# Performance work log

Measured on AMD Instinct MI355X. Metric: run time of the kernel, lower is better.

## Reference

```python
import jax, jax.numpy as jnp
import numpy as np

T, B, V, H = 512, 1024, 64, 100  # seq_len, batch, vocab(output_size), hidden_size


def setup_inputs() -> dict:
    key = jax.random.key(0)
    ks = jax.random.split(key, 9)
    s = 0.1
    x = jax.random.uniform(ks[0], (T, B, V), dtype=jnp.float32)  # teacher-forced inputs (one-hot-like floats)
    h = jax.random.normal(ks[1], (1, B, H), dtype=jnp.float32)   # encoder final hidden
    lens = jax.random.randint(ks[2], (B,), 1, T + 1, dtype=jnp.int32)
    lengths = jnp.sort(lens)[::-1]          # descending, packed-sequence order
    lengths = lengths.at[0].set(T)          # max length == T (batch_sizes[0] == B)
    W_ih = jax.random.normal(ks[3], (3 * H, V), dtype=jnp.float32) * s
    W_hh = jax.random.normal(ks[4], (3 * H, H), dtype=jnp.float32) * s
    b_ih = jax.random.normal(ks[5], (3 * H,), dtype=jnp.float32) * s
    b_hh = jax.random.normal(ks[6], (3 * H,), dtype=jnp.float32) * s
    W_out = jax.random.normal(ks[7], (V, H), dtype=jnp.float32) * s
    b_out = jax.random.normal(ks[8], (V,), dtype=jnp.float32) * s
    return dict(x=x, h=h, lengths=lengths, W_ih=W_ih, W_hh=W_hh,
                b_ih=b_ih, b_hh=b_hh, W_out=W_out, b_out=b_out)


def gru_cell(x_t, h_t, W_ih, W_hh, b_ih, b_hh):
    # PyTorch nn.GRUCell math, gate order (r, z, n)
    gi = x_t @ W_ih.T + b_ih   # [B, 3H]
    gh = h_t @ W_hh.T + b_hh   # [B, 3H]
    i_r, i_z, i_n = jnp.split(gi, 3, axis=-1)
    h_r, h_z, h_n = jnp.split(gh, 3, axis=-1)
    r = jax.nn.sigmoid(i_r + h_r)
    z = jax.nn.sigmoid(i_z + h_z)
    n = jnp.tanh(i_n + r * h_n)
    return (1.0 - z) * n + z * h_t


def reference(x, h, lengths, W_ih, W_hh, b_ih, b_hh, W_out, b_out):
    # Packed-sequence GRUCell decode with full teacher forcing (forcing_ratio=1.0).
    # Padded emulation: at step t only rows with t < length are active
    # (== first batch_sizes[t] rows in packed order since lengths are descending).
    hidden0 = h[0]                                          # [B, H]
    mask = jnp.arange(T)[:, None] < lengths[None, :]        # [T, B]

    def step(hidden, inp):
        x_t, m = inp
        h_new = gru_cell(x_t, hidden, W_ih, W_hh, b_ih, b_hh)
        hidden = jnp.where(m[:, None], h_new, hidden)
        logp = jax.nn.log_softmax(hidden @ W_out.T + b_out, axis=-1)  # [B, V]
        return hidden, jnp.where(m[:, None], logp, 0.0)

    _, outputs = jax.lax.scan(step, hidden0, (x, mask))
    return outputs  # [T, B, V] log-probs, zero at padded positions
```

## Files before the change

kernel.cpp:

```cpp
#include <hip/hip_runtime.h>


#define T_STEPS 512
#define BATCH   1024
#define VOCAB   64
#define HID     100
#define BB      16
#define NKH     4
#define NKX     2
#define HSTR    136
#define LSTR    68

typedef _Float16 f16;
typedef _Float16 f16x8 __attribute__((ext_vector_type(8)));
typedef float    f32x4 __attribute__((ext_vector_type(4)));

#define MFMA(A_, B_, C_) __builtin_amdgcn_mfma_f32_16x16x32_f16((A_), (B_), (C_), 0, 0, 0)

__device__ __forceinline__ float sigm(float v)   { return 1.0f / (1.0f + __expf(-v)); }
__device__ __forceinline__ float tanh_f(float v) { return 1.0f - 2.0f / (__expf(2.0f * v) + 1.0f); }

__global__ __launch_bounds__(512, 2) void gru_mfma(
    const float* __restrict__ x, const float* __restrict__ h0,
    const int* __restrict__ lengths,
    const float* __restrict__ W_ih, const float* __restrict__ W_hh,
    const float* __restrict__ b_ih, const float* __restrict__ b_hh,
    const float* __restrict__ W_out, const float* __restrict__ b_out,
    float* __restrict__ out)
{
    const int tid = threadIdx.x;
    const int w   = tid >> 6;
    const int l   = tid & 63;
    const int c   = l & 15;
    const int lg  = l >> 4;
    const int rowbase = blockIdx.x * BB;

    __shared__ alignas(16) f16   hHi[2][BB * HSTR];
    __shared__ alignas(16) f16   hLo[2][BB * HSTR];
    __shared__ alignas(16) float logitsL[BB * LSTR];
    __shared__ int lensL[BB];

    f16x8 wf[18];
    float bin = 0.f;
    float hold4[4];
    int   lenv[4];

    #pragma unroll
    for (int r = 0; r < 4; ++r) lenv[r] = lengths[rowbase + lg * 4 + r];

    if (w < 7) {
        const int gl = 16 * w + c;
        const bool gv = gl < HID;
        #pragma unroll
        for (int s = 0; s < 3; ++s) {
            const int g = s * HID + gl;
            #pragma unroll
            for (int ks = 0; ks < NKH; ++ks) {
                f16x8 v;
                #pragma unroll
                for (int j = 0; j < 8; ++j) {
                    const int k = ks * 32 + lg * 8 + j;
                    float val = 0.f;
                    if (gv) {
                        if (k < HID)        val = W_hh[(size_t)g * HID + k];
                        else if (k == HID)  val = (s < 2) ? (b_ih[g] + b_hh[g]) : b_hh[g];
                    }
                    v[j] = (f16)val;
                }
                wf[s * 4 + ks] = v;
            }
            #pragma unroll
            for (int ks = 0; ks < NKX; ++ks) {
                f16x8 v;
                #pragma unroll
                for (int j = 0; j < 8; ++j) {
                    const int k = ks * 32 + lg * 8 + j;
                    v[j] = (f16)(gv ? W_ih[(size_t)g * VOCAB + k] : 0.f);
                }
                wf[12 + s * 2 + ks] = v;
            }
        }
        bin = gv ? b_ih[2 * HID + gl] : 0.f;

        #pragma unroll
        for (int r = 0; r < 4; ++r) {
            const int row = lg * 4 + r;
            float hv = gv ? h0[(size_t)(rowbase + row) * HID + gl] : 0.f;
            hold4[r] = hv;
            if (gv) {
                f16 hi = (f16)hv;
                hHi[0][row * HSTR + gl] = hi;
                hLo[0][row * HSTR + gl] = (f16)(hv - (float)hi);
            }
        }
    } else {
        #pragma unroll
        for (int vt = 0; vt < 4; ++vt) {
            const int vr = 16 * vt + c;
            #pragma unroll
            for (int ks = 0; ks < NKH; ++ks) {
                f16x8 v;
                #pragma unroll
                for (int j = 0; j < 8; ++j) {
                    const int k = ks * 32 + lg * 8 + j;
                    float val = 0.f;
                    if (k < HID)        val = W_out[(size_t)vr * HID + k];
                    else if (k == HID)  val = b_out[vr];
                    v[j] = (f16)val;
                }
                wf[vt * 4 + ks] = v;
            }
        }
        hold4[0] = hold4[1] = hold4[2] = hold4[3] = 0.f;
    }

    if (tid < BB) {
        lensL[tid] = lengths[rowbase + tid];
        #pragma unroll
        for (int k = HID; k < 128; ++k) {
            hHi[0][tid * HSTR + k] = (f16)0.f;  hLo[0][tid * HSTR + k] = (f16)0.f;
            hHi[1][tid * HSTR + k] = (f16)0.f;  hLo[1][tid * HSTR + k] = (f16)0.f;
        }
        hHi[0][tid * HSTR + HID] = (f16)1.0f;
        hHi[1][tid * HSTR + HID] = (f16)1.0f;
    }

    f16x8 xf[NKX];
    if (w < 7) {
        const float* xp = x + ((size_t)rowbase + c) * VOCAB + lg * 8;
        #pragma unroll
        for (int ks = 0; ks < NKX; ++ks) {
            float4 a  = *reinterpret_cast<const float4*>(xp + ks * 32);
            float4 b2 = *reinterpret_cast<const float4*>(xp + ks * 32 + 4);
            f16x8 v;
            v[0] = (f16)a.x;  v[1] = (f16)a.y;  v[2] = (f16)a.z;  v[3] = (f16)a.w;
            v[4] = (f16)b2.x; v[5] = (f16)b2.y; v[6] = (f16)b2.z; v[7] = (f16)b2.w;
            xf[ks] = v;
        }
    }
    __syncthreads();

    for (int t = 0; t <= T_STEPS; ++t) {
        const int cur = t & 1;
        if (w < 7) {
            if (t < T_STEPS) {
                const int tn = (t + 1 < T_STEPS) ? t + 1 : t;
                const float* xp = x + ((size_t)tn * BATCH + rowbase + c) * VOCAB + lg * 8;
                float4 xp0 = *reinterpret_cast<const float4*>(xp);
                float4 xp1 = *reinterpret_cast<const float4*>(xp + 4);
                float4 xp2 = *reinterpret_cast<const float4*>(xp + 32);
                float4 xp3 = *reinterpret_cast<const float4*>(xp + 36);

                f16x8 hh[NKH], hl[NKH];
                #pragma unroll
                for (int ks = 0; ks < NKH; ++ks) {
                    const int off = c * HSTR + ks * 32 + lg * 8;
                    hh[ks] = *reinterpret_cast<const f16x8*>(&hHi[cur][off]);
                    hl[ks] = *reinterpret_cast<const f16x8*>(&hLo[cur][off]);
                }

                f32x4 aR = {0.f,0.f,0.f,0.f}, aZ = aR, aNX = aR, aNH = aR;
                #pragma unroll
                for (int ks = 0; ks < NKX; ++ks) {
                    aR  = MFMA(xf[ks], wf[12 + ks], aR);
                    aZ  = MFMA(xf[ks], wf[14 + ks], aZ);
                    aNX = MFMA(xf[ks], wf[16 + ks], aNX);
                }
                #pragma unroll
                for (int ks = 0; ks < NKH; ++ks) {
                    aR  = MFMA(hl[ks], wf[0 + ks], aR);
                    aR  = MFMA(hh[ks], wf[0 + ks], aR);
                    aZ  = MFMA(hl[ks], wf[4 + ks], aZ);
                    aZ  = MFMA(hh[ks], wf[4 + ks], aZ);
                    aNH = MFMA(hl[ks], wf[8 + ks], aNH);
                    aNH = MFMA(hh[ks], wf[8 + ks], aNH);
                }

                const int kk = 16 * w + c;
                const bool kv = kk < HID;
                #pragma unroll
                for (int r = 0; r < 4; ++r) {
                    float rg   = sigm(aR[r]);
                    float zg   = sigm(aZ[r]);
                    float ng   = tanh_f(fmaf(rg, aNH[r], aNX[r] + bin));
                    float hnew = fmaf(zg, hold4[r] - ng, ng);
                    float hv   = (t < lenv[r]) ? hnew : hold4[r];
                    hold4[r] = hv;
                    if (kv) {
                        const int row = lg * 4 + r;
                        f16 hi = (f16)hv;
                        hHi[cur ^ 1][row * HSTR + kk] = hi;
                        hLo[cur ^ 1][row * HSTR + kk] = (f16)(hv - (float)hi);
                    }
                }

                f16x8 v;
                v[0] = (f16)xp0.x; v[1] = (f16)xp0.y; v[2] = (f16)xp0.z; v[3] = (f16)xp0.w;
                v[4] = (f16)xp1.x; v[5] = (f16)xp1.y; v[6] = (f16)xp1.z; v[7] = (f16)xp1.w;
                xf[0] = v;
                v[0] = (f16)xp2.x; v[1] = (f16)xp2.y; v[2] = (f16)xp2.z; v[3] = (f16)xp2.w;
                v[4] = (f16)xp3.x; v[5] = (f16)xp3.y; v[6] = (f16)xp3.z; v[7] = (f16)xp3.w;
                xf[1] = v;
            }
        } else {
            if (t > 0) {
                const int tp = t - 1;
                f16x8 hh[NKH], hl[NKH];
                #pragma unroll
                for (int ks = 0; ks < NKH; ++ks) {
                    const int off = c * HSTR + ks * 32 + lg * 8;
                    hh[ks] = *reinterpret_cast<const f16x8*>(&hHi[cur][off]);
                    hl[ks] = *reinterpret_cast<const f16x8*>(&hLo[cur][off]);
                }
                f32x4 acc0 = {0.f,0.f,0.f,0.f}, acc1 = acc0, acc2 = acc0, acc3 = acc0;
                #pragma unroll
                for (int ks = 0; ks < NKH; ++ks) {
                    acc0 = MFMA(hl[ks], wf[0  + ks], acc0);
                    acc0 = MFMA(hh[ks], wf[0  + ks], acc0);
                    acc1 = MFMA(hl[ks], wf[4  + ks], acc1);
                    acc1 = MFMA(hh[ks], wf[4  + ks], acc1);
                    acc2 = MFMA(hl[ks], wf[8  + ks], acc2);
                    acc2 = MFMA(hh[ks], wf[8  + ks], acc2);
                    acc3 = MFMA(hl[ks], wf[12 + ks], acc3);
                    acc3 = MFMA(hh[ks], wf[12 + ks], acc3);
                }
                #pragma unroll
                for (int r = 0; r < 4; ++r) {
                    float m = fmaxf(fmaxf(acc0[r], acc1[r]), fmaxf(acc2[r], acc3[r]));
                    #pragma unroll
                    for (int off = 8; off >= 1; off >>= 1) m = fmaxf(m, __shfl_xor(m, off));
                    float s = __expf(acc0[r] - m) + __expf(acc1[r] - m)
                            + __expf(acc2[r] - m) + __expf(acc3[r] - m);
                    #pragma unroll
                    for (int off = 8; off >= 1; off >>= 1) s += __shfl_xor(s, off);
                    float ls = m + __logf(s);
                    const int row = lg * 4 + r;
                    logitsL[row * LSTR +      c] = acc0[r] - ls;
                    logitsL[row * LSTR + 16 + c] = acc1[r] - ls;
                    logitsL[row * LSTR + 32 + c] = acc2[r] - ls;
                    logitsL[row * LSTR + 48 + c] = acc3[r] - ls;
                }
                #pragma unroll
                for (int j = 0; j < 4; ++j) {
                    const int row4 = 4 * j + lg;
                    float4 v4 = *reinterpret_cast<const float4*>(&logitsL[row4 * LSTR + c * 4]);
                    if (tp >= lensL[row4]) v4 = make_float4(0.f, 0.f, 0.f, 0.f);
                    *reinterpret_cast<float4*>(
                        out + ((size_t)tp * BATCH + rowbase + row4) * VOCAB + c * 4) = v4;
                }
            }
        }
        __syncthreads();
    }
}

extern "C" void kernel_launch(void* const* d_in, const int* in_sizes, int n_in,
                              void* d_out, int out_size, void* d_ws, size_t ws_size,
                              hipStream_t stream) {
    const float* x     = (const float*)d_in[0];
    const float* h0    = (const float*)d_in[1];
    const int*   lens  = (const int*)  d_in[2];
    const float* W_ih  = (const float*)d_in[3];
    const float* W_hh  = (const float*)d_in[4];
    const float* b_ih  = (const float*)d_in[5];
    const float* b_hh  = (const float*)d_in[6];
    const float* W_out = (const float*)d_in[7];
    const float* b_out = (const float*)d_in[8];
    float* outp = (float*)d_out;

    gru_mfma<<<BATCH / BB, 512, 0, stream>>>(x, h0, lens, W_ih, W_hh,
                                             b_ih, b_hh, W_out, b_out, outp);
}
```

Baseline: 1.097 ms.

## Split MFMA accumulator chains, write logits directly, use lighter LDS-only barrier

Splits the hi/lo MFMA accumulation into independent accumulators so the dependent chains are shorter, and moves the x conversion earlier. The logits stage now writes scalar outputs straight to global memory instead of staging them through LDS and issuing float4 stores. The per-step barrier is replaced with a barrier that waits only on LDS counters, skipping the wait for global stores. Fast reciprocal intrinsics replace divisions in the activation functions. Direct scalar stores are less coalesced than the float4 path, and the added accumulators raise register use.

```diff
diff --git a/kernel.cpp b/kernel.cpp
--- a/kernel.cpp
+++ b/kernel.cpp
@@ -9,7 +9,6 @@
 #define NKH     4
 #define NKX     2
 #define HSTR    136
-#define LSTR    68
 
 typedef _Float16 f16;
 typedef _Float16 f16x8 __attribute__((ext_vector_type(8)));
@@ -17,8 +16,16 @@
 
 #define MFMA(A_, B_, C_) __builtin_amdgcn_mfma_f32_16x16x32_f16((A_), (B_), (C_), 0, 0, 0)
 
-__device__ __forceinline__ float sigm(float v)   { return 1.0f / (1.0f + __expf(-v)); }
-__device__ __forceinline__ float tanh_f(float v) { return 1.0f - 2.0f / (__expf(2.0f * v) + 1.0f); }
+__device__ __forceinline__ float rcp_f(float v)  { return __builtin_amdgcn_rcpf(v); }
+__device__ __forceinline__ float sigm(float v)   { return rcp_f(1.0f + __expf(-v)); }
+__device__ __forceinline__ float tanh_f(float v) { return 1.0f - 2.0f * rcp_f(__expf(2.0f * v) + 1.0f); }
+
+__device__ __forceinline__ void sync_lds() {
+    __builtin_amdgcn_sched_barrier(0);
+    asm volatile("s_waitcnt lgkmcnt(0)" ::: "memory");
+    __builtin_amdgcn_s_barrier();
+    __builtin_amdgcn_sched_barrier(0);
+}
 
 __global__ __launch_bounds__(512, 2) void gru_mfma(
     const float* __restrict__ x, const float* __restrict__ h0,
@@ -35,10 +42,8 @@
     const int lg  = l >> 4;
     const int rowbase = blockIdx.x * BB;
 
-    __shared__ alignas(16) f16   hHi[2][BB * HSTR];
-    __shared__ alignas(16) f16   hLo[2][BB * HSTR];
-    __shared__ alignas(16) float logitsL[BB * LSTR];
-    __shared__ int lensL[BB];
+    __shared__ alignas(16) f16 hHi[2][BB * HSTR];
+    __shared__ alignas(16) f16 hLo[2][BB * HSTR];
 
     f16x8 wf[18];
     float bin = 0.f;
@@ -115,7 +120,6 @@
     }
 
     if (tid < BB) {
-        lensL[tid] = lengths[rowbase + tid];
         #pragma unroll
         for (int k = HID; k < 128; ++k) {
             hHi[0][tid * HSTR + k] = (f16)0.f;  hLo[0][tid * HSTR + k] = (f16)0.f;
@@ -159,30 +163,42 @@
                     hl[ks] = *reinterpret_cast<const f16x8*>(&hLo[cur][off]);
                 }
 
-                f32x4 aR = {0.f,0.f,0.f,0.f}, aZ = aR, aNX = aR, aNH = aR;
+                f32x4 zz = {0.f, 0.f, 0.f, 0.f};
+                f32x4 aRa = zz, aZa = zz, aNX = zz;
+                f32x4 aRb = zz, aZb = zz, aNHa = zz, aNHb = zz;
                 #pragma unroll
                 for (int ks = 0; ks < NKX; ++ks) {
-                    aR  = MFMA(xf[ks], wf[12 + ks], aR);
-                    aZ  = MFMA(xf[ks], wf[14 + ks], aZ);
+                    aRa = MFMA(xf[ks], wf[12 + ks], aRa);
+                    aZa = MFMA(xf[ks], wf[14 + ks], aZa);
                     aNX = MFMA(xf[ks], wf[16 + ks], aNX);
                 }
                 #pragma unroll
                 for (int ks = 0; ks < NKH; ++ks) {
-                    aR  = MFMA(hl[ks], wf[0 + ks], aR);
-                    aR  = MFMA(hh[ks], wf[0 + ks], aR);
-                    aZ  = MFMA(hl[ks], wf[4 + ks], aZ);
-                    aZ  = MFMA(hh[ks], wf[4 + ks], aZ);
-                    aNH = MFMA(hl[ks], wf[8 + ks], aNH);
-                    aNH = MFMA(hh[ks], wf[8 + ks], aNH);
+                    aRa  = MFMA(hh[ks], wf[0 + ks], aRa);
+                    aRb  = MFMA(hl[ks], wf[0 + ks], aRb);
+                    aZa  = MFMA(hh[ks], wf[4 + ks], aZa);
+                    aZb  = MFMA(hl[ks], wf[4 + ks], aZb);
+                    aNHa = MFMA(hh[ks], wf[8 + ks], aNHa);
+                    aNHb = MFMA(hl[ks], wf[8 + ks], aNHb);
+                }
+
+                {
+                    f16x8 v;
+                    v[0] = (f16)xp0.x; v[1] = (f16)xp0.y; v[2] = (f16)xp0.z; v[3] = (f16)xp0.w;
+                    v[4] = (f16)xp1.x; v[5] = (f16)xp1.y; v[6] = (f16)xp1.z; v[7] = (f16)xp1.w;
+                    xf[0] = v;
+                    v[0] = (f16)xp2.x; v[1] = (f16)xp2.y; v[2] = (f16)xp2.z; v[3] = (f16)xp2.w;
+                    v[4] = (f16)xp3.x; v[5] = (f16)xp3.y; v[6] = (f16)xp3.z; v[7] = (f16)xp3.w;
+                    xf[1] = v;
                 }
 
                 const int kk = 16 * w + c;
                 const bool kv = kk < HID;
                 #pragma unroll
                 for (int r = 0; r < 4; ++r) {
-                    float rg   = sigm(aR[r]);
-                    float zg   = sigm(aZ[r]);
-                    float ng   = tanh_f(fmaf(rg, aNH[r], aNX[r] + bin));
+                    float rg   = sigm(aRa[r] + aRb[r]);
+                    float zg   = sigm(aZa[r] + aZb[r]);
+                    float ng   = tanh_f(fmaf(rg, aNHa[r] + aNHb[r], aNX[r] + bin));
                     float hnew = fmaf(zg, hold4[r] - ng, ng);
                     float hv   = (t < lenv[r]) ? hnew : hold4[r];
                     hold4[r] = hv;
@@ -193,14 +209,6 @@
                         hLo[cur ^ 1][row * HSTR + kk] = (f16)(hv - (float)hi);
                     }
                 }
-
-                f16x8 v;
-                v[0] = (f16)xp0.x; v[1] = (f16)xp0.y; v[2] = (f16)xp0.z; v[3] = (f16)xp0.w;
-                v[4] = (f16)xp1.x; v[5] = (f16)xp1.y; v[6] = (f16)xp1.z; v[7] = (f16)xp1.w;
-                xf[0] = v;
-                v[0] = (f16)xp2.x; v[1] = (f16)xp2.y; v[2] = (f16)xp2.z; v[3] = (f16)xp2.w;
-                v[4] = (f16)xp3.x; v[5] = (f16)xp3.y; v[6] = (f16)xp3.z; v[7] = (f16)xp3.w;
-                xf[1] = v;
             }
         } else {
             if (t > 0) {
@@ -212,45 +220,44 @@
                     hh[ks] = *reinterpret_cast<const f16x8*>(&hHi[cur][off]);
                     hl[ks] = *reinterpret_cast<const f16x8*>(&hLo[cur][off]);
                 }
-                f32x4 acc0 = {0.f,0.f,0.f,0.f}, acc1 = acc0, acc2 = acc0, acc3 = acc0;
-                #pragma unroll
-                for (int ks = 0; ks < NKH; ++ks) {
-                    acc0 = MFMA(hl[ks], wf[0  + ks], acc0);
-                    acc0 = MFMA(hh[ks], wf[0  + ks], acc0);
-                    acc1 = MFMA(hl[ks], wf[4  + ks], acc1);
-                    acc1 = MFMA(hh[ks], wf[4  + ks], acc1);
-                    acc2 = MFMA(hl[ks], wf[8  + ks], acc2);
-                    acc2 = MFMA(hh[ks], wf[8  + ks], acc2);
-                    acc3 = MFMA(hl[ks], wf[12 + ks], acc3);
-                    acc3 = MFMA(hh[ks], wf[12 + ks], acc3);
+                f32x4 zz = {0.f, 0.f, 0.f, 0.f};
+                f32x4 a0h = zz, a1h = zz, a2h = zz, a3h = zz;
+                f32x4 a0l = zz, a1l = zz, a2l = zz, a3l = zz;
+                #pragma unroll
+                for (int ks = 0; ks < NKH; ++ks) {
+                    a0h = MFMA(hh[ks], wf[0  + ks], a0h);
+                    a0l = MFMA(hl[ks], wf[0  + ks], a0l);
+                    a1h = MFMA(hh[ks], wf[4  + ks], a1h);
+                    a1l = MFMA(hl[ks], wf[4  + ks], a1l);
+                    a2h = MFMA(hh[ks], wf[8  + ks], a2h);
+                    a2l = MFMA(hl[ks], wf[8  + ks], a2l);
+                    a3h = MFMA(hh[ks], wf[12 + ks], a3h);
+                    a3l = MFMA(hl[ks], wf[12 + ks], a3l);
                 }
                 #pragma unroll
                 for (int r = 0; r < 4; ++r) {
-                    float m = fmaxf(fmaxf(acc0[r], acc1[r]), fmaxf(acc2[r], acc3[r]));
+                    float v0 = a0h[r] + a0l[r];
+                    float v1 = a1h[r] + a1l[r];
+                    float v2 = a2h[r] + a2l[r];
+                    float v3 = a3h[r] + a3l[r];
+                    float m = fmaxf(fmaxf(v0, v1), fmaxf(v2, v3));
                     #pragma unroll
                     for (int off = 8; off >= 1; off >>= 1) m = fmaxf(m, __shfl_xor(m, off));
-                    float s = __expf(acc0[r] - m) + __expf(acc1[r] - m)
-                            + __expf(acc2[r] - m) + __expf(acc3[r] - m);
+                    float s = __expf(v0 - m) + __expf(v1 - m)
+                            + __expf(v2 - m) + __expf(v3 - m);
                     #pragma unroll
                     for (int off = 8; off >= 1; off >>= 1) s += __shfl_xor(s, off);
                     float ls = m + __logf(s);
-                    const int row = lg * 4 + r;
-                    logitsL[row * LSTR +      c] = acc0[r] - ls;
-                    logitsL[row * LSTR + 16 + c] = acc1[r] - ls;
-                    logitsL[row * LSTR + 32 + c] = acc2[r] - ls;
-                    logitsL[row * LSTR + 48 + c] = acc3[r] - ls;
-                }
-                #pragma unroll
-                for (int j = 0; j < 4; ++j) {
-                    const int row4 = 4 * j + lg;
-                    float4 v4 = *reinterpret_cast<const float4*>(&logitsL[row4 * LSTR + c * 4]);
-                    if (tp >= lensL[row4]) v4 = make_float4(0.f, 0.f, 0.f, 0.f);
-                    *reinterpret_cast<float4*>(
-                        out + ((size_t)tp * BATCH + rowbase + row4) * VOCAB + c * 4) = v4;
-                }
-            }
-        }
-        __syncthreads();
+                    const bool act = tp < lenv[r];
+                    float* orow = out + ((size_t)tp * BATCH + rowbase + lg * 4 + r) * VOCAB + c;
+                    orow[ 0] = act ? (v0 - ls) : 0.f;
+                    orow[16] = act ? (v1 - ls) : 0.f;
+                    orow[32] = act ? (v2 - ls) : 0.f;
+                    orow[48] = act ? (v3 - ls) : 0.f;
+                }
+            }
+        }
+        sync_lds();
     }
 }
 
```

Result: no change. 1.077 ms (-1.8%).
